# Kernel optimization log

Hardware: AMD Instinct MI355X
Metric: run time of the kernel (lower is better)

The kernel has to match this reference:

```python
import jax, jax.numpy as jnp
import numpy as np

NUM_HEADS = 12
WIN = 7  # window_size[0] == window_size[1]


def setup_inputs() -> dict:
    key = jax.random.key(0)
    ks = jax.random.split(key, 8)
    B_, N, C = 2048, WIN * WIN, 384
    nW = 64
    return {
        "x": jax.random.normal(ks[0], (B_, N, C), dtype=jnp.float32),
        "mask": jax.random.normal(ks[1], (nW, N, N), dtype=jnp.float32),
        "qkv_w": jax.random.normal(ks[2], (3 * C, C), dtype=jnp.float32) * 0.02,
        "qkv_b": jax.random.normal(ks[3], (3 * C,), dtype=jnp.float32) * 0.02,
        "proj_w": jax.random.normal(ks[4], (C, C), dtype=jnp.float32) * 0.02,
        "proj_b": jax.random.normal(ks[5], (C,), dtype=jnp.float32) * 0.02,
        "rpb_table": jax.random.normal(ks[6], ((2 * WIN - 1) ** 2, NUM_HEADS), dtype=jnp.float32) * 0.02,
        "rel_index": jax.random.randint(ks[7], (N * N,), 0, (2 * WIN - 1) ** 2, dtype=jnp.int32),
    }


def reference(x, mask, qkv_w, qkv_b, proj_w, proj_b, rpb_table, rel_index):
    B_, N, C = x.shape
    H = NUM_HEADS
    d = C // H
    scale = d ** -0.5

    # QKV projection (quant wrappers act as identity in non-quant state)
    qkv = x @ qkv_w.T + qkv_b                      # [B_, N, 3C]
    qkv = qkv.reshape(B_, N, 3, H, d).transpose(2, 0, 3, 1, 4)  # [3, B_, H, N, d]
    q, k, v = qkv[0], qkv[1], qkv[2]

    attn = jnp.einsum("bhnd,bhmd->bhnm", q * scale, k)  # [B_, H, N, N]

    # relative position bias gather: [N*N] -> [N, N, H] -> [H, N, N]
    bias = rpb_table[rel_index].reshape(N, N, H).transpose(2, 0, 1)
    attn = attn + bias[None]

    # shifted-window mask add
    nW = mask.shape[0]
    attn = attn.reshape(B_ // nW, nW, H, N, N) + mask[None, :, None]
    attn = attn.reshape(B_, H, N, N)

    attn = jax.nn.softmax(attn, axis=-1)

    out = jnp.einsum("bhnm,bhmd->bhnd", attn, v)   # [B_, H, N, d]
    out = out.transpose(0, 2, 1, 3).reshape(B_, N, C)
    out = out @ proj_w.T + proj_b
    return out, attn
```

## Files before the change

kernel.cpp:

```cpp
#include <hip/hip_runtime.h>
#include <hip/hip_bf16.h>
#include <stdint.h>

#define H_ 12
#define D_ 32
#define N_ 49
#define C_ 384
#define B_TOT 2048
#define BH 24576
#define M_ROWS 100352
#define SCALE 0.17677669529663689f

typedef float f32x4 __attribute__((ext_vector_type(4)));
typedef __bf16 bf16x8 __attribute__((ext_vector_type(8)));
typedef unsigned short ushortx8 __attribute__((ext_vector_type(8)));

static __device__ __forceinline__ unsigned short f2bf(float f) {
  __bf16 b = (__bf16)f;
  return __builtin_bit_cast(unsigned short, b);
}

static __device__ __forceinline__ uint4 pack8(float4 a, float4 b) {
  ushortx8 v;
  v[0] = f2bf(a.x); v[1] = f2bf(a.y); v[2] = f2bf(a.z); v[3] = f2bf(a.w);
  v[4] = f2bf(b.x); v[5] = f2bf(b.y); v[6] = f2bf(b.z); v[7] = f2bf(b.w);
  return __builtin_bit_cast(uint4, v);
}

#define GL16(gp, lp)                                                        \
  __builtin_amdgcn_global_load_lds(                                         \
      (const __attribute__((address_space(1))) unsigned int*)(gp),          \
      (__attribute__((address_space(3))) unsigned int*)(lp), 16, 0, 0)

__global__ void prep(const float* __restrict__ wq, const float* __restrict__ wpw,
                     const float* __restrict__ mask, const float* __restrict__ rpb,
                     const int* __restrict__ ridx,
                     unsigned short* __restrict__ wq_bf,
                     unsigned short* __restrict__ wp_bf,
                     float* __restrict__ comb) {
  const int blk = blockIdx.x, tid = threadIdx.x;
  if (blk < 216) {
    const int i = blk * 256 + tid;
    float4 a = ((const float4*)wq)[2 * i];
    float4 b = ((const float4*)wq)[2 * i + 1];
    *(uint4*)&wq_bf[(size_t)i * 8] = pack8(a, b);
  } else if (blk < 288) {
    const int i = (blk - 216) * 256 + tid;
    float4 a = ((const float4*)wpw)[2 * i];
    float4 b = ((const float4*)wpw)[2 * i + 1];
    *(uint4*)&wp_bf[(size_t)i * 8] = pack8(a, b);
  } else {
    const int wh = blk - 288;
    const int w = wh / 12, h = wh - w * 12;
    float* cb = comb + (size_t)wh * 4096;
    const float* mw = mask + (size_t)w * N_ * N_;
    for (int e = tid; e < 4096; e += 256) {
      const int r = e >> 6, c = e & 63;
      float v;
      if (c >= N_) v = -1e30f;
      else if (r >= N_) v = 0.0f;
      else v = mw[r * N_ + c] + rpb[ridx[r * N_ + c] * H_ + h];
      cb[e] = v;
    }
  }
}

__global__ __launch_bounds__(256, 3)
void qkv_gemm(const float* __restrict__ A,
              const unsigned short* __restrict__ W,
              const float* __restrict__ bias, unsigned short* __restrict__ qkv) {
  __shared__ __align__(16) unsigned short smem[16384];
  const int tid = threadIdx.x;
  const int w = blockIdx.x;
  const int t = (w & 7) * 882 + (w >> 3);
  const int bm = t / 9, bn = t - bm * 9;
  const int lane = tid & 63, wv = tid >> 6;
  const int wm = wv >> 1, wn = wv & 1;
  const int lo = lane & 15, hi = lane >> 4;

  const int arow = tid >> 1, acg = tid & 1;
  const int ac0 = (acg * 2) ^ ((arow >> 1) & 3);
  const int ac1 = (acg * 2 + 1) ^ ((arow >> 1) & 3);
  const int sr0 = tid >> 2, sq0 = (tid & 3) ^ ((sr0 >> 1) & 3);
  const int ci1 = tid + 256;
  const int sr1 = ci1 >> 2, sq1 = (ci1 & 3) ^ ((sr1 >> 1) & 3);

  const float* Ab = A + (size_t)bm * 128 * 384 + arow * 384 + acg * 16;
  const unsigned short* Wb = W + (size_t)bn * 128 * 384;

  f32x4 acc[4][4];
#pragma unroll
  for (int i = 0; i < 4; i++)
#pragma unroll
    for (int j = 0; j < 4; j++)
#pragma unroll
      for (int r = 0; r < 4; r++) acc[i][j][r] = 0.0f;

  {
    float4 s0 = *(const float4*)(Ab + 0);
    float4 s1 = *(const float4*)(Ab + 4);
    float4 s2 = *(const float4*)(Ab + 8);
    float4 s3 = *(const float4*)(Ab + 12);
    GL16(Wb + sr0 * 384 + sq0 * 8, smem + 4096 + tid * 8);
    GL16(Wb + sr1 * 384 + sq1 * 8, smem + 4096 + ci1 * 8);
    *(uint4*)&smem[(arow * 4 + ac0) * 8] = pack8(s0, s1);
    *(uint4*)&smem[(arow * 4 + ac1) * 8] = pack8(s2, s3);
  }
  __syncthreads();

  int buf = 0;
  for (int kt = 0; kt < 12; kt++) {
    float4 s0, s1, s2, s3;
    if (kt < 11) {
      const int kk = (kt + 1) * 32;
      s0 = *(const float4*)(Ab + kk + 0);
      s1 = *(const float4*)(Ab + kk + 4);
      s2 = *(const float4*)(Ab + kk + 8);
      s3 = *(const float4*)(Ab + kk + 12);
      unsigned short* nb = smem + (buf ^ 1) * 8192;
      GL16(Wb + sr0 * 384 + kk + sq0 * 8, nb + 4096 + tid * 8);
      GL16(Wb + sr1 * 384 + kk + sq1 * 8, nb + 4096 + ci1 * 8);
    }
    const unsigned short* ba = smem + buf * 8192;
    bf16x8 af[4], bfm[4];
#pragma unroll
    for (int mt = 0; mt < 4; mt++) {
      const int row = wm * 64 + mt * 16 + lo;
      af[mt] = *(const bf16x8*)&ba[(row * 4 + (hi ^ ((row >> 1) & 3))) * 8];
    }
#pragma unroll
    for (int nt = 0; nt < 4; nt++) {
      const int row = wn * 64 + nt * 16 + lo;
      bfm[nt] = *(const bf16x8*)&ba[4096 + (row * 4 + (hi ^ ((row >> 1) & 3))) * 8];
    }
#pragma unroll
    for (int mt = 0; mt < 4; mt++)
#pragma unroll
      for (int nt = 0; nt < 4; nt++)
        acc[mt][nt] = __builtin_amdgcn_mfma_f32_16x16x32_bf16(af[mt], bfm[nt], acc[mt][nt], 0, 0, 0);
    if (kt < 11) {
      unsigned short* nb = smem + (buf ^ 1) * 8192;
      *(uint4*)&nb[(arow * 4 + ac0) * 8] = pack8(s0, s1);
      *(uint4*)&nb[(arow * 4 + ac1) * 8] = pack8(s2, s3);
    }
    __syncthreads();
    buf ^= 1;
  }

  unsigned short* ep = smem + wv * 4096;
#pragma unroll
  for (int nt = 0; nt < 4; nt++) {
    const int j = bn * 128 + wn * 64 + nt * 16 + lo;
    const float bj = bias[j];
    const float mul = (j < 384) ? SCALE : 1.0f;
    const int c16 = nt * 2 + (lo >> 3);
    const int wi = lo & 7;
#pragma unroll
    for (int mt = 0; mt < 4; mt++) {
#pragma unroll
      for (int r = 0; r < 4; r++) {
        const int row = mt * 16 + hi * 4 + r;
        ep[row * 64 + ((c16 ^ hi) << 3) + wi] = f2bf((acc[mt][nt][r] + bj) * mul);
      }
    }
  }
#pragma unroll
  for (int cc = 0; cc < 2; cc++) {
    const int cidx = cc * 64 + lane;
    const int lr = cidx >> 1, lch = cidx & 1;
    const int i = bm * 128 + wm * 64 + lr;
    const int b = i / 49, sq = i - b * 49;
    const int j0 = bn * 128 + wn * 64 + lch * 32;
    const int which = j0 / 384;
    const int rem = j0 - which * 384;
    const int h = rem >> 5;
    const int hlr = (lr >> 2) & 3;
    unsigned short* dst = qkv + ((size_t)which * BH + (size_t)b * H_ + h) * (N_ * D_) + sq * D_;
#pragma unroll
    for (int q = 0; q < 4; q++) {
      const int c16r = lch * 4 + q;
      *(uint4*)(dst + q * 8) = *(const uint4*)&ep[lr * 64 + ((c16r ^ hlr) << 3)];
    }
  }
}

__global__ __launch_bounds__(64, 2)
void attn_kernel(const unsigned short* __restrict__ qkv,
                 const float* __restrict__ comb,
                 float* __restrict__ probs,
                 unsigned short* __restrict__ av) {
  __shared__ __align__(16) unsigned short P[64 * 64];
  __shared__ __align__(16) unsigned short VT[32 * 64];
  const int lane = threadIdx.x;
  const int lo = lane & 15, hi = lane >> 4;
  const int l7 = lo & 7;
  const int h = blockIdx.x, b = blockIdx.y;

  const unsigned short* qp = qkv + (size_t)(b * H_ + h) * (N_ * D_);
  const unsigned short* kp = qp + (size_t)BH * (N_ * D_);
  const unsigned short* vp = kp + (size_t)BH * (N_ * D_);

  {
    unsigned int* vz = (unsigned int*)VT;
#pragma unroll
    for (int i = 0; i < 16; i++) vz[lane + 64 * i] = 0u;
  }
  __syncthreads();

  bf16x8 aq[4], bk[4];
#pragma unroll
  for (int t = 0; t < 4; t++) {
    aq[t] = *(const bf16x8*)(qp + (t * 16 + lo) * D_ + hi * 8);
    bk[t] = *(const bf16x8*)(kp + (t * 16 + lo) * D_ + hi * 8);
  }
  f32x4 s[4][4];
#pragma unroll
  for (int mt = 0; mt < 4; mt++)
#pragma unroll
    for (int nt = 0; nt < 4; nt++) {
#pragma unroll
      for (int r = 0; r < 4; r++) s[mt][nt][r] = 0.0f;
      s[mt][nt] = __builtin_amdgcn_mfma_f32_16x16x32_bf16(aq[mt], bk[nt], s[mt][nt], 0, 0, 0);
    }

#pragma unroll
  for (int it = 0; it < 4; it++) {
    const int idx = it * 64 + lane;
    if (idx < 196) {
      const int sq = idx >> 2, ch = idx & 3;
      ushortx8 vv = *(const ushortx8*)(vp + sq * D_ + ch * 8);
#pragma unroll
      for (int jj = 0; jj < 8; jj++)
        VT[(ch * 8 + jj) * 64 + (((sq >> 3) ^ jj) << 3) + (sq & 7)] = vv[jj];
    }
  }

  const float* cb = comb + (size_t)((b & 63) * H_ + h) * 4096;
#pragma unroll
  for (int mt = 0; mt < 4; mt++) {
#pragma unroll
    for (int r = 0; r < 4; r++) {
      const int row = mt * 16 + hi * 4 + r;
      const float* crow = cb + row * 64 + lo;
      float v0 = s[mt][0][r] + crow[0];
      float v1 = s[mt][1][r] + crow[16];
      float v2 = s[mt][2][r] + crow[32];
      float v3 = s[mt][3][r] + crow[48];
      float m = fmaxf(fmaxf(v0, v1), fmaxf(v2, v3));
      m = fmaxf(m, __shfl_xor(m, 1));
      m = fmaxf(m, __shfl_xor(m, 2));
      m = fmaxf(m, __shfl_xor(m, 4));
      m = fmaxf(m, __shfl_xor(m, 8));
      v0 = __expf(v0 - m); v1 = __expf(v1 - m);
      v2 = __expf(v2 - m); v3 = __expf(v3 - m);
      float sum = v0 + v1 + v2 + v3;
      sum += __shfl_xor(sum, 1);
      sum += __shfl_xor(sum, 2);
      sum += __shfl_xor(sum, 4);
      sum += __shfl_xor(sum, 8);
      const float rinv = 1.0f / sum;
      s[mt][0][r] = v0 * rinv; s[mt][1][r] = v1 * rinv;
      s[mt][2][r] = v2 * rinv; s[mt][3][r] = v3 * rinv;
    }
  }

  const size_t pbase = (size_t)(b * H_ + h) * N_ * N_;
#pragma unroll
  for (int mt = 0; mt < 4; mt++) {
#pragma unroll
    for (int r = 0; r < 4; r++) {
      const int row = mt * 16 + hi * 4 + r;
      if (row < N_) {
#pragma unroll
        for (int nt = 0; nt < 4; nt++) {
          const int c = nt * 16 + lo;
          if (c < N_) probs[pbase + row * N_ + c] = s[mt][nt][r];
        }
      }
      const int r7 = row & 7;
#pragma unroll
      for (int nt = 0; nt < 4; nt++)
        P[row * 64 + (((nt * 2 + (lo >> 3)) ^ r7) << 3) + l7] = f2bf(s[mt][nt][r]);
    }
  }
  __syncthreads();

  f32x4 o[4][2];
#pragma unroll
  for (int mt = 0; mt < 4; mt++)
#pragma unroll
    for (int n2 = 0; n2 < 2; n2++)
#pragma unroll
      for (int r = 0; r < 4; r++) o[mt][n2][r] = 0.0f;
#pragma unroll
  for (int ks = 0; ks < 2; ks++) {
    bf16x8 pa[4], vb[2];
#pragma unroll
    for (int mt = 0; mt < 4; mt++)
      pa[mt] = *(const bf16x8*)&P[(mt * 16 + lo) * 64 + (((ks * 4 + hi) ^ l7) << 3)];
#pragma unroll
    for (int n2 = 0; n2 < 2; n2++)
      vb[n2] = *(const bf16x8*)&VT[(n2 * 16 + lo) * 64 + (((ks * 4 + hi) ^ l7) << 3)];
#pragma unroll
    for (int mt = 0; mt < 4; mt++)
#pragma unroll
      for (int n2 = 0; n2 < 2; n2++)
        o[mt][n2] = __builtin_amdgcn_mfma_f32_16x16x32_bf16(pa[mt], vb[n2], o[mt][n2], 0, 0, 0);
  }

  __syncthreads();
#pragma unroll
  for (int mt = 0; mt < 4; mt++) {
#pragma unroll
    for (int r = 0; r < 4; r++) {
      const int row = mt * 16 + hi * 4 + r;
      if (row < N_) {
#pragma unroll
        for (int n2 = 0; n2 < 2; n2++)
          P[row * 40 + n2 * 16 + lo] = f2bf(o[mt][n2][r]);
      }
    }
  }
  if (lane < N_) {
    unsigned short* dst = av + ((size_t)b * N_ + lane) * C_ + h * D_;
    const unsigned short* src = P + lane * 40;
#pragma unroll
    for (int q = 0; q < 4; q++)
      *(uint4*)(dst + q * 8) = *(const uint4*)(src + q * 8);
  }
}

__global__ __launch_bounds__(256, 4)
void proj_gemm(const unsigned short* __restrict__ A,
               const unsigned short* __restrict__ W,
               const float* __restrict__ bias, float* __restrict__ out) {
  __shared__ __align__(16) unsigned short smem[16384];
  const int tid = threadIdx.x;
  const int w = blockIdx.x;
  const int t = (w & 7) * 294 + (w >> 3);
  const int bm = t / 3, bn = t - bm * 3;
  const int lane = tid & 63, wv = tid >> 6;
  const int wm = wv >> 1, wn = wv & 1;
  const int lo = lane & 15, hi = lane >> 4;

  const int sr0 = tid >> 2, sq0 = (tid & 3) ^ ((sr0 >> 1) & 3);
  const int ci1 = tid + 256;
  const int sr1 = ci1 >> 2, sq1 = (ci1 & 3) ^ ((sr1 >> 1) & 3);

  const unsigned short* Ab = A + (size_t)bm * 128 * 384;
  const unsigned short* Wb = W + (size_t)bn * 128 * 384;

  f32x4 acc[4][4];
#pragma unroll
  for (int i = 0; i < 4; i++)
#pragma unroll
    for (int j = 0; j < 4; j++)
#pragma unroll
      for (int r = 0; r < 4; r++) acc[i][j][r] = 0.0f;

  {
    unsigned short* b0 = smem;
    GL16(Ab + sr0 * 384 + sq0 * 8, b0 + tid * 8);
    GL16(Ab + sr1 * 384 + sq1 * 8, b0 + ci1 * 8);
    GL16(Wb + sr0 * 384 + sq0 * 8, b0 + 4096 + tid * 8);
    GL16(Wb + sr1 * 384 + sq1 * 8, b0 + 4096 + ci1 * 8);
  }
  __syncthreads();

  int buf = 0;
  for (int kt = 0; kt < 12; kt++) {
    if (kt < 11) {
      const int kk = (kt + 1) * 32;
      unsigned short* nb = smem + (buf ^ 1) * 8192;
      GL16(Ab + sr0 * 384 + kk + sq0 * 8, nb + tid * 8);
      GL16(Ab + sr1 * 384 + kk + sq1 * 8, nb + ci1 * 8);
      GL16(Wb + sr0 * 384 + kk + sq0 * 8, nb + 4096 + tid * 8);
      GL16(Wb + sr1 * 384 + kk + sq1 * 8, nb + 4096 + ci1 * 8);
    }
    const unsigned short* ba = smem + buf * 8192;
    bf16x8 af[4], bfm[4];
#pragma unroll
    for (int mt = 0; mt < 4; mt++) {
      const int row = wm * 64 + mt * 16 + lo;
      af[mt] = *(const bf16x8*)&ba[(row * 4 + (hi ^ ((row >> 1) & 3))) * 8];
    }
#pragma unroll
    for (int nt = 0; nt < 4; nt++) {
      const int row = wn * 64 + nt * 16 + lo;
      bfm[nt] = *(const bf16x8*)&ba[4096 + (row * 4 + (hi ^ ((row >> 1) & 3))) * 8];
    }
#pragma unroll
    for (int mt = 0; mt < 4; mt++)
#pragma unroll
      for (int nt = 0; nt < 4; nt++)
        acc[mt][nt] = __builtin_amdgcn_mfma_f32_16x16x32_bf16(af[mt], bfm[nt], acc[mt][nt], 0, 0, 0);
    __syncthreads();
    buf ^= 1;
  }

#pragma unroll
  for (int nt = 0; nt < 4; nt++) {
    const int j = bn * 128 + wn * 64 + nt * 16 + lo;
    const float bj = bias[j];
#pragma unroll
    for (int mt = 0; mt < 4; mt++) {
#pragma unroll
      for (int r = 0; r < 4; r++) {
        const int i = bm * 128 + wm * 64 + mt * 16 + hi * 4 + r;
        out[(size_t)i * 384 + j] = acc[mt][nt][r] + bj;
      }
    }
  }
}

extern "C" void kernel_launch(void* const* d_in, const int* in_sizes, int n_in,
                              void* d_out, int out_size, void* d_ws, size_t ws_size,
                              hipStream_t stream) {
  const float* x      = (const float*)d_in[0];
  const float* mask   = (const float*)d_in[1];
  const float* qkv_w  = (const float*)d_in[2];
  const float* qkv_b  = (const float*)d_in[3];
  const float* proj_w = (const float*)d_in[4];
  const float* proj_b = (const float*)d_in[5];
  const float* rpb    = (const float*)d_in[6];
  const int*   ridx   = (const int*)d_in[7];

  unsigned short* qkv   = (unsigned short*)d_ws;
  unsigned short* av    = qkv + (size_t)3 * BH * N_ * D_;
  float* comb           = (float*)(av + (size_t)M_ROWS * C_);
  unsigned short* wq_bf = (unsigned short*)(comb + 768 * 4096);
  unsigned short* wp_bf = wq_bf + 1152 * 384;
  float* out   = (float*)d_out;
  float* probs = out + (size_t)M_ROWS * C_;

  prep<<<1056, 256, 0, stream>>>(qkv_w, proj_w, mask, rpb, ridx,
                                 wq_bf, wp_bf, comb);
  qkv_gemm<<<7056, 256, 0, stream>>>(x, wq_bf, qkv_b, qkv);
  attn_kernel<<<dim3(H_, B_TOT), 64, 0, stream>>>(qkv, comb, probs, av);
  proj_gemm<<<2352, 256, 0, stream>>>(av, wp_bf, proj_b, out);
}
```

Baseline: 511.8 us.

## Stage fp32 activations via direct global-to-LDS loads and vectorize bias reads

After: 468.3 us. 8.5% less time.

```diff
diff --git a/kernel.cpp b/kernel.cpp
--- a/kernel.cpp
+++ b/kernel.cpp
@@ -60,7 +60,7 @@
       if (c >= N_) v = -1e30f;
       else if (r >= N_) v = 0.0f;
       else v = mw[r * N_ + c] + rpb[ridx[r * N_ + c] * H_ + h];
-      cb[e] = v;
+      cb[(r * 16 + (c & 15)) * 4 + (c >> 4)] = v;
     }
   }
 }
@@ -69,7 +69,7 @@
 void qkv_gemm(const float* __restrict__ A,
               const unsigned short* __restrict__ W,
               const float* __restrict__ bias, unsigned short* __restrict__ qkv) {
-  __shared__ __align__(16) unsigned short smem[16384];
+  __shared__ __align__(16) unsigned char smem[49152];
   const int tid = threadIdx.x;
   const int w = blockIdx.x;
   const int t = (w & 7) * 882 + (w >> 3);
@@ -78,14 +78,18 @@
   const int wm = wv >> 1, wn = wv & 1;
   const int lo = lane & 15, hi = lane >> 4;
 
-  const int arow = tid >> 1, acg = tid & 1;
-  const int ac0 = (acg * 2) ^ ((arow >> 1) & 3);
-  const int ac1 = (acg * 2 + 1) ^ ((arow >> 1) & 3);
+  int arow[4], agc[4];
+#pragma unroll
+  for (int q = 0; q < 4; q++) {
+    const int s = tid + 256 * q;
+    arow[q] = s >> 3;
+    agc[q] = (s & 7) ^ (arow[q] & 7);
+  }
   const int sr0 = tid >> 2, sq0 = (tid & 3) ^ ((sr0 >> 1) & 3);
   const int ci1 = tid + 256;
   const int sr1 = ci1 >> 2, sq1 = (ci1 & 3) ^ ((sr1 >> 1) & 3);
 
-  const float* Ab = A + (size_t)bm * 128 * 384 + arow * 384 + acg * 16;
+  const float* Ab = A + (size_t)bm * 128 * 384;
   const unsigned short* Wb = W + (size_t)bn * 128 * 384;
 
   f32x4 acc[4][4];
@@ -97,57 +101,57 @@
       for (int r = 0; r < 4; r++) acc[i][j][r] = 0.0f;
 
   {
-    float4 s0 = *(const float4*)(Ab + 0);
-    float4 s1 = *(const float4*)(Ab + 4);
-    float4 s2 = *(const float4*)(Ab + 8);
-    float4 s3 = *(const float4*)(Ab + 12);
-    GL16(Wb + sr0 * 384 + sq0 * 8, smem + 4096 + tid * 8);
-    GL16(Wb + sr1 * 384 + sq1 * 8, smem + 4096 + ci1 * 8);
-    *(uint4*)&smem[(arow * 4 + ac0) * 8] = pack8(s0, s1);
-    *(uint4*)&smem[(arow * 4 + ac1) * 8] = pack8(s2, s3);
+#pragma unroll
+    for (int q = 0; q < 4; q++)
+      GL16(Ab + arow[q] * 384 + agc[q] * 4, smem + (tid + 256 * q) * 16);
+    GL16(Wb + sr0 * 384 + sq0 * 8, smem + 32768 + tid * 16);
+    GL16(Wb + sr1 * 384 + sq1 * 8, smem + 32768 + ci1 * 16);
   }
   __syncthreads();
 
   int buf = 0;
   for (int kt = 0; kt < 12; kt++) {
-    float4 s0, s1, s2, s3;
     if (kt < 11) {
       const int kk = (kt + 1) * 32;
-      s0 = *(const float4*)(Ab + kk + 0);
-      s1 = *(const float4*)(Ab + kk + 4);
-      s2 = *(const float4*)(Ab + kk + 8);
-      s3 = *(const float4*)(Ab + kk + 12);
-      unsigned short* nb = smem + (buf ^ 1) * 8192;
-      GL16(Wb + sr0 * 384 + kk + sq0 * 8, nb + 4096 + tid * 8);
-      GL16(Wb + sr1 * 384 + kk + sq1 * 8, nb + 4096 + ci1 * 8);
-    }
-    const unsigned short* ba = smem + buf * 8192;
+      unsigned char* na = smem + (buf ^ 1) * 16384;
+      unsigned char* nbv = smem + 32768 + (buf ^ 1) * 8192;
+#pragma unroll
+      for (int q = 0; q < 4; q++)
+        GL16(Ab + arow[q] * 384 + kk + agc[q] * 4, na + (tid + 256 * q) * 16);
+      GL16(Wb + sr0 * 384 + kk + sq0 * 8, nbv + tid * 16);
+      GL16(Wb + sr1 * 384 + kk + sq1 * 8, nbv + ci1 * 16);
+    }
+    const float* fa = (const float*)(smem + buf * 16384);
+    const unsigned short* fb = (const unsigned short*)(smem + 32768 + buf * 8192);
     bf16x8 af[4], bfm[4];
 #pragma unroll
     for (int mt = 0; mt < 4; mt++) {
       const int row = wm * 64 + mt * 16 + lo;
-      af[mt] = *(const bf16x8*)&ba[(row * 4 + (hi ^ ((row >> 1) & 3))) * 8];
+      const int r7 = row & 7;
+      f32x4 a0 = *(const f32x4*)&fa[row * 32 + (((2 * hi) ^ r7) << 2)];
+      f32x4 a1 = *(const f32x4*)&fa[row * 32 + (((2 * hi + 1) ^ r7) << 2)];
+      bf16x8 v;
+      v[0] = (__bf16)a0[0]; v[1] = (__bf16)a0[1];
+      v[2] = (__bf16)a0[2]; v[3] = (__bf16)a0[3];
+      v[4] = (__bf16)a1[0]; v[5] = (__bf16)a1[1];
+      v[6] = (__bf16)a1[2]; v[7] = (__bf16)a1[3];
+      af[mt] = v;
     }
 #pragma unroll
     for (int nt = 0; nt < 4; nt++) {
       const int row = wn * 64 + nt * 16 + lo;
-      bfm[nt] = *(const bf16x8*)&ba[4096 + (row * 4 + (hi ^ ((row >> 1) & 3))) * 8];
+      bfm[nt] = *(const bf16x8*)&fb[(row * 4 + (hi ^ ((row >> 1) & 3))) * 8];
     }
 #pragma unroll
     for (int mt = 0; mt < 4; mt++)
 #pragma unroll
       for (int nt = 0; nt < 4; nt++)
         acc[mt][nt] = __builtin_amdgcn_mfma_f32_16x16x32_bf16(af[mt], bfm[nt], acc[mt][nt], 0, 0, 0);
-    if (kt < 11) {
-      unsigned short* nb = smem + (buf ^ 1) * 8192;
-      *(uint4*)&nb[(arow * 4 + ac0) * 8] = pack8(s0, s1);
-      *(uint4*)&nb[(arow * 4 + ac1) * 8] = pack8(s2, s3);
-    }
     __syncthreads();
     buf ^= 1;
   }
 
-  unsigned short* ep = smem + wv * 4096;
+  unsigned short* ep = (unsigned short*)smem + wv * 4096;
 #pragma unroll
   for (int nt = 0; nt < 4; nt++) {
     const int j = bn * 128 + wn * 64 + nt * 16 + lo;
@@ -241,11 +245,11 @@
 #pragma unroll
     for (int r = 0; r < 4; r++) {
       const int row = mt * 16 + hi * 4 + r;
-      const float* crow = cb + row * 64 + lo;
-      float v0 = s[mt][0][r] + crow[0];
-      float v1 = s[mt][1][r] + crow[16];
-      float v2 = s[mt][2][r] + crow[32];
-      float v3 = s[mt][3][r] + crow[48];
+      const float4 cr = *(const float4*)(cb + (row * 16 + lo) * 4);
+      float v0 = s[mt][0][r] + cr.x;
+      float v1 = s[mt][1][r] + cr.y;
+      float v2 = s[mt][2][r] + cr.z;
+      float v3 = s[mt][3][r] + cr.w;
       float m = fmaxf(fmaxf(v0, v1), fmaxf(v2, v3));
       m = fmaxf(m, __shfl_xor(m, 1));
       m = fmaxf(m, __shfl_xor(m, 2));
```
